# Performance work log

Hardware: AMD Instinct MI355X
Metric: run time of the kernel (lower is better)

## Reference

```python
import jax, jax.numpy as jnp
import numpy as np

N = 20000      # nodes
E = 320000     # edges (avg degree 16)
C = 64         # channels per degree
H = 8          # attention heads
DIM1 = 3       # degree-1 representation dim (2*1+1)
NUM_FEATURES = C * 1 + C * 3  # key_fiber.num_features = 256


def setup_inputs() -> dict:
    key = jax.random.key(0)
    ks = jax.random.split(key, 7)
    return {
        "value_0": jax.random.normal(ks[0], (E, C, 1), dtype=jnp.float32),
        "value_1": jax.random.normal(ks[1], (E, C, DIM1), dtype=jnp.float32),
        "key_0": jax.random.normal(ks[2], (E, C, 1), dtype=jnp.float32),
        "key_1": jax.random.normal(ks[3], (E, C, DIM1), dtype=jnp.float32),
        "query_0": jax.random.normal(ks[4], (N, C, 1), dtype=jnp.float32),
        "query_1": jax.random.normal(ks[5], (N, C, DIM1), dtype=jnp.float32),
        "dst": jax.random.randint(ks[6], (E,), 0, N),
    }


def _to_heads(f0, f1):
    # Fiber.to_attention_heads: per degree [n, C, dim] -> [n, H, (C//H)*dim], concat on last dim
    n = f0.shape[0]
    return jnp.concatenate([f0.reshape(n, H, -1), f1.reshape(n, H, -1)], axis=-1)


def reference(value_0, value_1, key_0, key_1, query_0, query_1, dst):
    k = _to_heads(key_0, key_1)        # [E, H, Dk]
    q = _to_heads(query_0, query_1)    # [N, H, Dk]
    # dgl.ops.e_dot_v: dot edge key with destination-node query, then scale
    logits = jnp.einsum('ehd,ehd->eh', k, q[dst]) / np.float32(np.sqrt(NUM_FEATURES))
    edge_prelogits = logits            # returned pre-softmax (scaled) as in original
    # edge_softmax over incoming edges of each destination node, per head
    m = jax.ops.segment_max(logits, dst, num_segments=N)           # [N, H]
    w = jnp.exp(logits - m[dst])                                   # [E, H]
    denom = jax.ops.segment_sum(w, dst, num_segments=N)            # [N, H]
    alpha = w / denom[dst]                                         # [E, H]

    def agg(v, dim):
        # value view: [E, H, C//H, dim]; weighted copy_e_sum -> [N, C, dim]
        vh = v.reshape(E, H, C // H, dim)
        out = jax.ops.segment_sum(alpha[:, :, None, None] * vh, dst, num_segments=N)
        return out.reshape(N, C, dim)

    out_0 = agg(value_0, 1)
    out_1 = agg(value_1, DIM1)
    return out_0, out_1, edge_prelogits
```

## Files before the change

kernel.cpp:

```cpp
#include <hip/hip_runtime.h>

#define N_NODES 20000
#define N_EDGES 320000
#define SLOTS  48


#define DOT4(a,b) ((a).x*(b).x + (a).y*(b).y + (a).z*(b).z + (a).w*(b).w)
#define FMA4(a,s,p) { (a).x += (s)*(p).x; (a).y += (s)*(p).y; (a).z += (s)*(p).z; (a).w += (s)*(p).w; }

__global__ __launch_bounds__(256) void k_zero(int* __restrict__ p, int n)
{
    int i = blockIdx.x * 256 + threadIdx.x;
    if (i < n) p[i] = 0;
}

__global__ __launch_bounds__(256) void k_fill(
    const int* __restrict__ dst, int* __restrict__ counts, int* __restrict__ bucket)
{
    int e = blockIdx.x * 256 + threadIdx.x;
    if (e >= N_EDGES) return;
    int d = dst[e];
    int cnt = atomicAdd(&counts[d], 1);
    if (cnt < SLOTS) bucket[d * SLOTS + cnt] = e;
}

__global__ __launch_bounds__(256) void k_fused(
    const float* __restrict__ v0, const float* __restrict__ v1,
    const float* __restrict__ k0, const float* __restrict__ k1,
    const float* __restrict__ q0, const float* __restrict__ q1,
    const int* __restrict__ counts, const int* __restrict__ bucket,
    float* __restrict__ logits, float* __restrict__ out0, float* __restrict__ out1)
{
    int w = threadIdx.x >> 6, l = threadIdx.x & 63;
    int node = blockIdx.x * 4 + w;
    int deg = min(counts[node], SLOTS);
    const int* bk = bucket + node * SLOTS;

    int j = l >> 3, h = l & 7;
    bool lo = (j < 2);
    int koff = lo ? (h * 8 + 4 * j) : (h * 24 + 4 * (j - 2));
    int hv = (l < 16) ? (l >> 1) : (l - 16) / 6;

    float4 q4 = lo ? *(const float4*)(q0 + (size_t)node * 64  + koff)
                   : *(const float4*)(q1 + (size_t)node * 192 + koff);

    int eReg = (l < deg) ? bk[l] : 0;

    float S = 0.f;
    float4 acc = {0, 0, 0, 0};

#pragma unroll 2
    for (int i = 0; i < deg; i += 2) {
        int iB = min(i + 1, deg - 1);
        bool okB = (i + 1) < deg;
        int eA = __shfl(eReg, i);
        int eB = __shfl(eReg, iB);

        float4 kA = lo ? *(const float4*)(k0 + (size_t)eA * 64  + koff)
                       : *(const float4*)(k1 + (size_t)eA * 192 + koff);
        float4 kB = lo ? *(const float4*)(k0 + (size_t)eB * 64  + koff)
                       : *(const float4*)(k1 + (size_t)eB * 192 + koff);
        float4 vA = (l < 16) ? ((const float4*)(v0 + (size_t)eA * 64))[l]
                             : ((const float4*)(v1 + (size_t)eA * 192))[l - 16];
        float4 vB = (l < 16) ? ((const float4*)(v0 + (size_t)eB * 64))[l]
                             : ((const float4*)(v1 + (size_t)eB * 192))[l - 16];

        float pA = DOT4(kA, q4);
        float pB = DOT4(kB, q4);
        pA += __shfl_xor(pA, 8);  pB += __shfl_xor(pB, 8);
        pA += __shfl_xor(pA, 16); pB += __shfl_xor(pB, 16);
        pA += __shfl_xor(pA, 32); pB += __shfl_xor(pB, 32);
        float xA = pA * 0.0625f;
        float xB = pB * 0.0625f;
        float exA = __expf(xA);
        float exB = okB ? __expf(xB) : 0.f;
        S += exA + exB;

        if (j == 0) {
            logits[(size_t)eA * 8 + h] = xA;
            if (okB) logits[(size_t)eB * 8 + h] = xB;
        }

        float aA = __shfl(exA, hv);
        float aB = __shfl(exB, hv);
        FMA4(acc, aA, vA);
        FMA4(acc, aB, vB);
    }

    float rinv = (S > 0.f) ? 1.f / S : 0.f;
    float rv = __shfl(rinv, hv);
    acc.x *= rv; acc.y *= rv; acc.z *= rv; acc.w *= rv;

    if (l < 16) ((float4*)(out0 + (size_t)node * 64))[l]       = acc;
    else        ((float4*)(out1 + (size_t)node * 192))[l - 16] = acc;
}

extern "C" void kernel_launch(void* const* d_in, const int* in_sizes, int n_in,
                              void* d_out, int out_size, void* d_ws, size_t ws_size,
                              hipStream_t stream) {
    const float* v0 = (const float*)d_in[0];
    const float* v1 = (const float*)d_in[1];
    const float* k0 = (const float*)d_in[2];
    const float* k1 = (const float*)d_in[3];
    const float* q0 = (const float*)d_in[4];
    const float* q1 = (const float*)d_in[5];
    const int*  dst = (const int*)d_in[6];

    float* out0   = (float*)d_out;
    float* out1   = out0 + (size_t)N_NODES * 64;
    float* logits = out1 + (size_t)N_NODES * 192;

    int* wsI    = (int*)d_ws;
    int* counts = wsI;
    int* bucket = wsI + 20000;

    k_zero  <<<79,   256, 0, stream>>>(counts, N_NODES);
    k_fill  <<<1250, 256, 0, stream>>>(dst, counts, bucket);
    k_fused <<<5000, 256, 0, stream>>>(v0, v1, k0, k1, q0, q1,
                                       counts, bucket, logits, out0, out1);
}
```

Baseline: 182.3 us.

## Software-pipeline edge gathers with triple-buffered register prefetch in fused attention kernel

```diff
diff --git a/kernel.cpp b/kernel.cpp
--- a/kernel.cpp
+++ b/kernel.cpp
@@ -22,6 +22,42 @@
     int d = dst[e];
     int cnt = atomicAdd(&counts[d], 1);
     if (cnt < SLOTS) bucket[d * SLOTS + cnt] = e;
+}
+
+#define LOADP(P, EA, EB, KA, KB, VA, VB)                                        \
+{                                                                               \
+    int iA = min(2 * (P), dm1);                                                 \
+    int iB = min(2 * (P) + 1, dm1);                                             \
+    EA = __shfl(eReg, iA);                                                      \
+    EB = __shfl(eReg, iB);                                                      \
+    KA = lo ? *(const float4*)(k0 + (size_t)EA * 64  + koff)                    \
+            : *(const float4*)(k1 + (size_t)EA * 192 + koff);                   \
+    KB = lo ? *(const float4*)(k0 + (size_t)EB * 64  + koff)                    \
+            : *(const float4*)(k1 + (size_t)EB * 192 + koff);                   \
+    VA = (l < 16) ? ((const float4*)(v0 + (size_t)EA * 64))[l]                  \
+                  : ((const float4*)(v1 + (size_t)EA * 192))[l - 16];           \
+    VB = (l < 16) ? ((const float4*)(v0 + (size_t)EB * 64))[l]                  \
+                  : ((const float4*)(v1 + (size_t)EB * 192))[l - 16];           \
+}
+
+#define CONSUME(P, EA, EB, KA, KB, VA, VB)                                      \
+{                                                                               \
+    bool okA = 2 * (P) < deg, okB = 2 * (P) + 1 < deg;                          \
+    float pA = DOT4(KA, q4), pB = DOT4(KB, q4);                                 \
+    pA += __shfl_xor(pA, 8);  pB += __shfl_xor(pB, 8);                          \
+    pA += __shfl_xor(pA, 16); pB += __shfl_xor(pB, 16);                         \
+    pA += __shfl_xor(pA, 32); pB += __shfl_xor(pB, 32);                         \
+    float xA = pA * 0.0625f, xB = pB * 0.0625f;                                 \
+    float exA = okA ? __expf(xA) : 0.f;                                         \
+    float exB = okB ? __expf(xB) : 0.f;                                         \
+    S += exA + exB;                                                             \
+    if (j == 0) {                                                               \
+        if (okA) logits[(size_t)EA * 8 + h] = xA;                               \
+        if (okB) logits[(size_t)EB * 8 + h] = xB;                               \
+    }                                                                           \
+    float aA = __shfl(exA, hv), aB = __shfl(exB, hv);                           \
+    FMA4(acc, aA, VA);                                                          \
+    FMA4(acc, aB, VB);                                                          \
 }
 
 __global__ __launch_bounds__(256) void k_fused(
@@ -49,42 +85,30 @@
     float S = 0.f;
     float4 acc = {0, 0, 0, 0};
 
-#pragma unroll 2
-    for (int i = 0; i < deg; i += 2) {
-        int iB = min(i + 1, deg - 1);
-        bool okB = (i + 1) < deg;
-        int eA = __shfl(eReg, i);
-        int eB = __shfl(eReg, iB);
+    int G = (deg + 1) >> 1;
+    int dm1 = (deg > 0) ? deg - 1 : 0;
 
-        float4 kA = lo ? *(const float4*)(k0 + (size_t)eA * 64  + koff)
-                       : *(const float4*)(k1 + (size_t)eA * 192 + koff);
-        float4 kB = lo ? *(const float4*)(k0 + (size_t)eB * 64  + koff)
-                       : *(const float4*)(k1 + (size_t)eB * 192 + koff);
-        float4 vA = (l < 16) ? ((const float4*)(v0 + (size_t)eA * 64))[l]
-                             : ((const float4*)(v1 + (size_t)eA * 192))[l - 16];
-        float4 vB = (l < 16) ? ((const float4*)(v0 + (size_t)eB * 64))[l]
-                             : ((const float4*)(v1 + (size_t)eB * 192))[l - 16];
+    float4 kA0, kB0, vA0, vB0, kA1, kB1, vA1, vB1, kA2, kB2, vA2, vB2;
+    int eA0, eB0, eA1, eB1, eA2, eB2;
 
-        float pA = DOT4(kA, q4);
-        float pB = DOT4(kB, q4);
-        pA += __shfl_xor(pA, 8);  pB += __shfl_xor(pB, 8);
-        pA += __shfl_xor(pA, 16); pB += __shfl_xor(pB, 16);
-        pA += __shfl_xor(pA, 32); pB += __shfl_xor(pB, 32);
-        float xA = pA * 0.0625f;
-        float xB = pB * 0.0625f;
-        float exA = __expf(xA);
-        float exB = okB ? __expf(xB) : 0.f;
-        S += exA + exB;
+    if (G > 0) {
+        LOADP(0, eA0, eB0, kA0, kB0, vA0, vB0);
+        if (G > 1) LOADP(1, eA1, eB1, kA1, kB1, vA1, vB1);
+        if (G > 2) LOADP(2, eA2, eB2, kA2, kB2, vA2, vB2);
 
-        if (j == 0) {
-            logits[(size_t)eA * 8 + h] = xA;
-            if (okB) logits[(size_t)eB * 8 + h] = xB;
+        int p = 0;
+#pragma unroll 1
+        for (; p + 3 < G; p += 3) {
+            CONSUME(p,     eA0, eB0, kA0, kB0, vA0, vB0);
+            LOADP(p + 3,   eA0, eB0, kA0, kB0, vA0, vB0);
+            CONSUME(p + 1, eA1, eB1, kA1, kB1, vA1, vB1);
+            LOADP(p + 4,   eA1, eB1, kA1, kB1, vA1, vB1);
+            CONSUME(p + 2, eA2, eB2, kA2, kB2, vA2, vB2);
+            LOADP(p + 5,   eA2, eB2, kA2, kB2, vA2, vB2);
         }
-
-        float aA = __shfl(exA, hv);
-        float aB = __shfl(exB, hv);
-        FMA4(acc, aA, vA);
-        FMA4(acc, aB, vB);
+        if (p < G)     CONSUME(p,     eA0, eB0, kA0, kB0, vA0, vB0);
+        if (p + 1 < G) CONSUME(p + 1, eA1, eB1, kA1, kB1, vA1, vB1);
+        if (p + 2 < G) CONSUME(p + 2, eA2, eB2, kA2, kB2, vA2, vB2);
     }
 
     float rinv = (S > 0.f) ? 1.f / S : 0.f;
```

Measured after the change: 179.4 us. About the same (-1.6%).

## Process each node with a 384-thread block, parallelizing edges across threads

Applied to the files above, without the earlier changes.

```diff
diff --git a/kernel.cpp b/kernel.cpp
--- a/kernel.cpp
+++ b/kernel.cpp
@@ -24,75 +24,92 @@
     if (cnt < SLOTS) bucket[d * SLOTS + cnt] = e;
 }
 
-__global__ __launch_bounds__(256) void k_fused(
+__global__ __launch_bounds__(384) void k_node(
     const float* __restrict__ v0, const float* __restrict__ v1,
     const float* __restrict__ k0, const float* __restrict__ k1,
     const float* __restrict__ q0, const float* __restrict__ q1,
     const int* __restrict__ counts, const int* __restrict__ bucket,
     float* __restrict__ logits, float* __restrict__ out0, float* __restrict__ out1)
 {
-    int w = threadIdx.x >> 6, l = threadIdx.x & 63;
-    int node = blockIdx.x * 4 + w;
+    __shared__ float Q[256];
+    __shared__ int   bkL[SLOTS];
+    __shared__ float P[SLOTS * 8];
+    __shared__ float wpart[6 * 8];
+    __shared__ float Rinv[8];
+    __shared__ float part[5 * 64 * 4];
+
+    int t = threadIdx.x;
+    int node = blockIdx.x;
     int deg = min(counts[node], SLOTS);
-    const int* bk = bucket + node * SLOTS;
 
-    int j = l >> 3, h = l & 7;
-    bool lo = (j < 2);
-    int koff = lo ? (h * 8 + 4 * j) : (h * 24 + 4 * (j - 2));
-    int hv = (l < 16) ? (l >> 1) : (l - 16) / 6;
+    if (t < 16)      ((float4*)Q)[t] = ((const float4*)(q0 + (size_t)node * 64))[t];
+    else if (t < 64) ((float4*)Q)[t] = ((const float4*)(q1 + (size_t)node * 192))[t - 16];
+    if (t < SLOTS) bkL[t] = bucket[node * SLOTS + t];
+    __syncthreads();
 
-    float4 q4 = lo ? *(const float4*)(q0 + (size_t)node * 64  + koff)
-                   : *(const float4*)(q1 + (size_t)node * 192 + koff);
+    int slot = t >> 3, h = t & 7;
+    float ex = 0.f;
+    if (slot < deg) {
+        int e = bkL[slot];
+        const float4* kr0 = (const float4*)(k0 + (size_t)e * 64  + h * 8);
+        const float4* kr1 = (const float4*)(k1 + (size_t)e * 192 + h * 24);
+        float4 K0 = kr0[0], K1 = kr0[1];
+        float4 K2 = kr1[0], K3 = kr1[1], K4 = kr1[2];
+        float4 K5 = kr1[3], K6 = kr1[4], K7 = kr1[5];
+        const float4* Qa = (const float4*)Q;
+        const float4* Qb = (const float4*)(Q + 64);
+        float4 A0 = Qa[h * 2], A1 = Qa[h * 2 + 1];
+        float4 B0 = Qb[h * 6], B1 = Qb[h * 6 + 1], B2 = Qb[h * 6 + 2];
+        float4 B3 = Qb[h * 6 + 3], B4 = Qb[h * 6 + 4], B5 = Qb[h * 6 + 5];
+        float x = DOT4(K0, A0) + DOT4(K1, A1)
+                + DOT4(K2, B0) + DOT4(K3, B1) + DOT4(K4, B2)
+                + DOT4(K5, B3) + DOT4(K6, B4) + DOT4(K7, B5);
+        x *= 0.0625f;
+        logits[(size_t)e * 8 + h] = x;
+        ex = __expf(x);
+        P[slot * 8 + h] = ex;
+    }
+    float s = ex;
+    s += __shfl_xor(s, 8);
+    s += __shfl_xor(s, 16);
+    s += __shfl_xor(s, 32);
+    if ((t & 63) < 8) wpart[(t >> 6) * 8 + h] = s;
+    __syncthreads();
+    if (t < 8) {
+        float S = 0.f;
+#pragma unroll
+        for (int i = 0; i < 6; ++i) S += wpart[i * 8 + t];
+        Rinv[t] = (S > 0.f) ? 1.f / S : 0.f;
+    }
+    __syncthreads();
 
-    int eReg = (l < deg) ? bk[l] : 0;
-
-    float S = 0.f;
+    int c4 = t & 63, sg = t >> 6;
+    int hv = (c4 < 16) ? (c4 >> 1) : (c4 - 16) / 6;
     float4 acc = {0, 0, 0, 0};
-
-#pragma unroll 2
-    for (int i = 0; i < deg; i += 2) {
-        int iB = min(i + 1, deg - 1);
-        bool okB = (i + 1) < deg;
-        int eA = __shfl(eReg, i);
-        int eB = __shfl(eReg, iB);
-
-        float4 kA = lo ? *(const float4*)(k0 + (size_t)eA * 64  + koff)
-                       : *(const float4*)(k1 + (size_t)eA * 192 + koff);
-        float4 kB = lo ? *(const float4*)(k0 + (size_t)eB * 64  + koff)
-                       : *(const float4*)(k1 + (size_t)eB * 192 + koff);
-        float4 vA = (l < 16) ? ((const float4*)(v0 + (size_t)eA * 64))[l]
-                             : ((const float4*)(v1 + (size_t)eA * 192))[l - 16];
-        float4 vB = (l < 16) ? ((const float4*)(v0 + (size_t)eB * 64))[l]
-                             : ((const float4*)(v1 + (size_t)eB * 192))[l - 16];
-
-        float pA = DOT4(kA, q4);
-        float pB = DOT4(kB, q4);
-        pA += __shfl_xor(pA, 8);  pB += __shfl_xor(pB, 8);
-        pA += __shfl_xor(pA, 16); pB += __shfl_xor(pB, 16);
-        pA += __shfl_xor(pA, 32); pB += __shfl_xor(pB, 32);
-        float xA = pA * 0.0625f;
-        float xB = pB * 0.0625f;
-        float exA = __expf(xA);
-        float exB = okB ? __expf(xB) : 0.f;
-        S += exA + exB;
-
-        if (j == 0) {
-            logits[(size_t)eA * 8 + h] = xA;
-            if (okB) logits[(size_t)eB * 8 + h] = xB;
+#pragma unroll
+    for (int r = 0; r < 8; ++r) {
+        int s2 = sg + 6 * r;
+        if (s2 < deg) {
+            int e = bkL[s2];
+            float a = P[s2 * 8 + hv];
+            float4 v4 = (c4 < 16) ? ((const float4*)(v0 + (size_t)e * 64))[c4]
+                                  : ((const float4*)(v1 + (size_t)e * 192))[c4 - 16];
+            FMA4(acc, a, v4);
         }
-
-        float aA = __shfl(exA, hv);
-        float aB = __shfl(exB, hv);
-        FMA4(acc, aA, vA);
-        FMA4(acc, aB, vB);
     }
-
-    float rinv = (S > 0.f) ? 1.f / S : 0.f;
-    float rv = __shfl(rinv, hv);
-    acc.x *= rv; acc.y *= rv; acc.z *= rv; acc.w *= rv;
-
-    if (l < 16) ((float4*)(out0 + (size_t)node * 64))[l]       = acc;
-    else        ((float4*)(out1 + (size_t)node * 192))[l - 16] = acc;
+    if (sg > 0) ((float4*)part)[(sg - 1) * 64 + c4] = acc;
+    __syncthreads();
+    if (sg == 0) {
+#pragma unroll
+        for (int i = 0; i < 5; ++i) {
+            float4 p = ((float4*)part)[i * 64 + c4];
+            acc.x += p.x; acc.y += p.y; acc.z += p.z; acc.w += p.w;
+        }
+        float rv = Rinv[hv];
+        acc.x *= rv; acc.y *= rv; acc.z *= rv; acc.w *= rv;
+        if (c4 < 16) ((float4*)(out0 + (size_t)node * 64))[c4]       = acc;
+        else         ((float4*)(out1 + (size_t)node * 192))[c4 - 16] = acc;
+    }
 }
 
 extern "C" void kernel_launch(void* const* d_in, const int* in_sizes, int n_in,
@@ -114,8 +131,8 @@
     int* counts = wsI;
     int* bucket = wsI + 20000;
 
-    k_zero  <<<79,   256, 0, stream>>>(counts, N_NODES);
-    k_fill  <<<1250, 256, 0, stream>>>(dst, counts, bucket);
-    k_fused <<<5000, 256, 0, stream>>>(v0, v1, k0, k1, q0, q1,
+    k_zero <<<79,    256, 0, stream>>>(counts, N_NODES);
+    k_fill <<<1250,  256, 0, stream>>>(dst, counts, bucket);
+    k_node <<<20000, 384, 0, stream>>>(v0, v1, k0, k1, q0, q1,
                                        counts, bucket, logits, out0, out1);
 }
```

Measured after the change: 190.6 us. +4.6%, slower.
